# Kernel tuning notes

Measured on AMD Instinct MI355X. Metric: run time of the kernel, lower is better.

The kernel has to match this reference:

```python
import jax, jax.numpy as jnp
import numpy as np

N, E = 50000, 800000
IN_DIM, H, OUT_DIM = 128, 32, 128


def _p(key, shape, fan_in):
    return jax.random.normal(key, shape, dtype=jnp.float32) / np.float32(np.sqrt(fan_in))


def gcn(x, edge_index, W, b):
    # GCNConv with DOUBLED self-loops (outer add_self_loops + gcn_norm's own):
    # deg[i] = in_degree(i) + 2, each node receives 2*dinv[i]^2 * h[i].
    src, dst = edge_index[0], edge_index[1]
    h = x @ W  # [N, out]
    deg = jnp.zeros((x.shape[0],), h.dtype).at[dst].add(1.0) + 2.0
    dinv = jax.lax.rsqrt(deg)
    coef = dinv[src] * dinv[dst]  # [E]
    agg = jax.ops.segment_sum(h[src] * coef[:, None], dst, num_segments=x.shape[0])
    agg = agg + (2.0 * dinv * dinv)[:, None] * h
    return agg + b


def multihop(x, edge_index, W, b, fW, fb):
    # hop loop in the source always re-uses initial_x -> collapses to 1 pass
    return gcn(x, edge_index, W, b) @ fW + fb


def deconv(xc, W, b):
    # ConvTranspose1d(kernel=2, stride=2): out[n,o,2l+t] = sum_c xc[n,c,l]*W[c,o,t] + b[o]
    y = jnp.einsum('ncl,cot->nolt', xc, W) + b[None, :, None, None]
    return y.reshape(y.shape[0], y.shape[1], -1)  # [N, O, 2L]


def setup_inputs() -> dict:
    key = jax.random.key(0)
    ks = jax.random.split(key, 30)
    return {
        'x': jax.random.normal(ks[0], (N, IN_DIM), jnp.float32),
        'edge_index': jax.random.randint(ks[1], (2, E), 0, N),
        'w_enc1': _p(ks[2], (IN_DIM, H), IN_DIM), 'b_enc1': _p(ks[3], (H,), H),
        'fw_enc1': _p(ks[4], (H, H), H), 'fb_enc1': _p(ks[5], (H,), H),
        'w_enc2': _p(ks[6], (H, 2 * H), H), 'b_enc2': _p(ks[7], (2 * H,), 2 * H),
        'fw_enc2': _p(ks[8], (2 * H, 2 * H), 2 * H), 'fb_enc2': _p(ks[9], (2 * H,), 2 * H),
        'w_enc3': _p(ks[10], (2 * H, 4 * H), 2 * H), 'b_enc3': _p(ks[11], (4 * H,), 4 * H),
        'fw_enc3': _p(ks[12], (4 * H, 4 * H), 4 * H), 'fb_enc3': _p(ks[13], (4 * H,), 4 * H),
        'wd1': _p(ks[14], (4 * H, 2 * H, 2), 4 * H), 'bd1': _p(ks[15], (2 * H,), 4 * H),
        'wd2': _p(ks[16], (2 * H, H, 2), 2 * H), 'bd2': _p(ks[17], (H,), 2 * H),
        'wd3': _p(ks[18], (H, H, 2), H), 'bd3': _p(ks[19], (H,), H),
        'ws1': _p(ks[20], (2 * H, 2 * H), 2 * H), 'bs1': _p(ks[21], (2 * H,), 2 * H),
        'ws2': _p(ks[22], (H, H), H), 'bs2': _p(ks[23], (H,), H),
        'wf': _p(ks[24], (8 * H, OUT_DIM), 8 * H), 'bf': _p(ks[25], (OUT_DIM,), 8 * H),
    }


def reference(x, edge_index, w_enc1, b_enc1, fw_enc1, fb_enc1,
              w_enc2, b_enc2, fw_enc2, fb_enc2,
              w_enc3, b_enc3, fw_enc3, fb_enc3,
              wd1, bd1, wd2, bd2, wd3, bd3,
              ws1, bs1, ws2, bs2, wf, bf):
    relu = jax.nn.relu
    x1 = relu(multihop(x, edge_index, w_enc1, b_enc1, fw_enc1, fb_enc1))   # [N, H]
    x2 = relu(multihop(x1, edge_index, w_enc2, b_enc2, fw_enc2, fb_enc2))  # [N, 2H]
    x3 = relu(multihop(x2, edge_index, w_enc3, b_enc3, fw_enc3, fb_enc3))  # [N, 4H]
    d = deconv(x3[:, :, None], wd1, bd1)            # [N, 2H, 2]
    s2 = x2 @ ws1 + bs1                              # skip_conv1 (k=1) == linear
    d = d + s2[:, :, None]                           # repeat over length
    d = deconv(d, wd2, bd2)                          # [N, H, 4]
    s1 = x1 @ ws2 + bs2
    d = d + s1[:, :, None]
    d = deconv(d, wd3, bd3)                          # [N, H, 8]
    out = d.reshape(d.shape[0], -1) @ wf + bf        # [N, OUT_DIM]
    return out
```

## Files before the change

### kernel.cpp

```cpp
#include <hip/hip_runtime.h>

#define NN 50000
#define NE 800000
#define NBLK 196
#define CAP 5120

typedef _Float16 half8 __attribute__((ext_vector_type(8)));
typedef _Float16 half4 __attribute__((ext_vector_type(4)));
typedef float f32x4v __attribute__((ext_vector_type(4)));

__launch_bounds__(256)
__global__ void k_A(const int* __restrict__ srcv, const int* __restrict__ dstv,
                    int* __restrict__ bcur, unsigned int* __restrict__ epk2,
                    const float* __restrict__ wd3, const float* __restrict__ wf,
                    const float* __restrict__ w2, const float* __restrict__ fw2,
                    const float* __restrict__ w3, const float* __restrict__ fw3,
                    const float* __restrict__ b1, const float* __restrict__ fw1,
                    const float* __restrict__ fb1,
                    const float* __restrict__ b2, const float* __restrict__ fb2,
                    const float* __restrict__ b3, const float* __restrict__ fb3,
                    float* __restrict__ G,
                    float* __restrict__ Wc2, float* __restrict__ Wc3,
                    float* __restrict__ bc1, float* __restrict__ bc2,
                    float* __restrict__ bc3,
                    const float* __restrict__ w1, _Float16* __restrict__ W1pk) {
  __shared__ int cnt[256];
  __shared__ int base[256];
  int t = threadIdx.x;
  int b = blockIdx.x;
  if (b < NBLK) {
    int e0 = b * 4096;
    cnt[t] = 0;
    __syncthreads();
    unsigned int pk[16];
    int lo[16], bk[16];
    bool ok[16];
#pragma unroll
    for (int i = 0; i < 16; ++i) {
      int e = e0 + i * 256 + t;
      ok[i] = (e < NE);
      if (ok[i]) {
        int s = srcv[e], d = dstv[e];
        bk[i] = d >> 8;
        pk[i] = (unsigned int)s | ((unsigned int)(d & 255) << 16);
        lo[i] = atomicAdd(&cnt[bk[i]], 1);
      }
    }
    __syncthreads();
    int c = cnt[t];
    if (c > 0) base[t] = atomicAdd(&bcur[t], c);
    __syncthreads();
#pragma unroll
    for (int i = 0; i < 16; ++i)
      if (ok[i]) epk2[(size_t)bk[i] * CAP + base[bk[i]] + lo[i]] = pk[i];
    return;
  }
  if (b < NBLK + 105) {
    int id = (b - NBLK) * 256 + t;
    if (id < 16384) {
      int k = id & 127, r = id >> 7;
      int c = r >> 2, l = r & 3;
      float s = 0.f;
      for (int o = 0; o < 32; ++o) {
        s = fmaf(wd3[c * 64 + o * 2 + 0], wf[(o * 8 + 2 * l + 0) * 128 + k], s);
        s = fmaf(wd3[c * 64 + o * 2 + 1], wf[(o * 8 + 2 * l + 1) * 128 + k], s);
      }
      G[r * 128 + k] = s;
      return;
    }
    int id2 = id - 16384;
    if (id2 < 2048) {
      int c = id2 >> 6, k = id2 & 63;
      float s = 0.f;
      for (int j = 0; j < 64; ++j) s = fmaf(w2[c * 64 + j], fw2[j * 64 + k], s);
      Wc2[id2] = s;
    } else if (id2 < 10240) {
      int idx = id2 - 2048;
      int c = idx >> 7, k = idx & 127;
      float s = 0.f;
      for (int j = 0; j < 128; ++j) s = fmaf(w3[c * 128 + j], fw3[j * 128 + k], s);
      Wc3[idx] = s;
    } else if (id2 < 10272) {
      int k = id2 - 10240;
      float s = fb1[k];
      for (int j = 0; j < 32; ++j) s = fmaf(b1[j], fw1[j * 32 + k], s);
      bc1[k] = s;
    } else if (id2 < 10336) {
      int k = id2 - 10272;
      float s = fb2[k];
      for (int j = 0; j < 64; ++j) s = fmaf(b2[j], fw2[j * 64 + k], s);
      bc2[k] = s;
    } else if (id2 < 10464) {
      int k = id2 - 10336;
      float s = fb3[k];
      for (int j = 0; j < 128; ++j) s = fmaf(b3[j], fw3[j * 128 + k], s);
      bc3[k] = s;
    }
    return;
  }
#pragma unroll
  for (int it = 0; it < 2; ++it) {
    int id = t + it * 256;
    int l = id & 63, f = id >> 6;
    int kb = f >> 1, nb = f & 1;
    int kbase = kb * 32 + ((l >> 4) << 3);
    int col = nb * 16 + (l & 15);
#pragma unroll
    for (int j = 0; j < 8; ++j)
      W1pk[id * 8 + j] = (_Float16)w1[(kbase + j) * 32 + col];
  }
}

__launch_bounds__(256)
__global__ void k_B(const unsigned int* __restrict__ epk2, const int* __restrict__ bcur,
                    int* __restrict__ row_start, int* __restrict__ bend,
                    float* __restrict__ dinv, float* __restrict__ rdinv,
                    unsigned short* __restrict__ esrc,
                    const float* __restrict__ wd2, const float* __restrict__ G,
                    const float* __restrict__ ws2,
                    float* __restrict__ Hm, float* __restrict__ A1) {
  int t = threadIdx.x;
  int b = blockIdx.x;
  if (b < NBLK) {
    __shared__ int cnt[256];
    __shared__ int cur[256];
    __shared__ int ss[256];
    int rs0 = b * CAP;
    int count = bcur[b];
    int rs1 = rs0 + count;
    cnt[t] = 0;
    __syncthreads();
    for (int i = rs0 + t; i < rs1; i += 256) {
      unsigned int p = epk2[i];
      atomicAdd(&cnt[(p >> 16) & 255], 1);
    }
    __syncthreads();
    int d = cnt[t];
    ss[t] = d;
    __syncthreads();
    for (int off = 1; off < 256; off <<= 1) {
      int v = (t >= off) ? ss[t - off] : 0;
      __syncthreads();
      ss[t] += v;
      __syncthreads();
    }
    int rs = rs0 + ss[t] - d;
    int node = b * 256 + t;
    if (node < NN) {
      row_start[node] = rs;
      float df = (float)d + 2.0f;
      dinv[node] = rsqrtf(df);
      rdinv[node] = sqrtf(df);
    }
    if (t == 0) bend[b] = rs1;
    if (b == 0 && t == 0) row_start[NN] = NBLK * CAP;
    cur[t] = rs;
    __syncthreads();
    for (int i = rs0 + t; i < rs1; i += 256) {
      unsigned int p = epk2[i];
      int dl = (p >> 16) & 255;
      int tgt = atomicAdd(&cur[dl], 1);
      esrc[tgt] = (unsigned short)(p & 0xFFFFu);
    }
    return;
  }
  int id = (b - NBLK) * 256 + t;
  if (id < 16384) {
    int k = id & 127, r = id >> 7;
    int c = r >> 1, l = r & 1;
    float s = 0.f;
    for (int o = 0; o < 32; ++o) {
      s = fmaf(wd2[c * 64 + o * 2 + 0], G[(o * 4 + 2 * l + 0) * 128 + k], s);
      s = fmaf(wd2[c * 64 + o * 2 + 1], G[(o * 4 + 2 * l + 1) * 128 + k], s);
    }
    Hm[r * 128 + k] = s;
  } else if (id < 16384 + 4096) {
    int idx = id - 16384;
    int k = idx & 127, c = idx >> 7;
    float s = 0.f;
    for (int o = 0; o < 32; ++o) {
      float g = G[(4 * o) * 128 + k] + G[(4 * o + 1) * 128 + k] +
                G[(4 * o + 2) * 128 + k] + G[(4 * o + 3) * 128 + k];
      s = fmaf(ws2[c * 32 + o], g, s);
    }
    A1[c * 128 + k] = s;
  }
}

__device__ inline half8 cvt8f(const float* __restrict__ p) {
  float4 u = *reinterpret_cast<const float4*>(p);
  float4 v = *reinterpret_cast<const float4*>(p + 4);
  half8 a;
  a[0] = (_Float16)u.x; a[1] = (_Float16)u.y; a[2] = (_Float16)u.z; a[3] = (_Float16)u.w;
  a[4] = (_Float16)v.x; a[5] = (_Float16)v.y; a[6] = (_Float16)v.z; a[7] = (_Float16)v.w;
  return a;
}

#define NG1 782
__launch_bounds__(256)
__global__ void k_C(const float* __restrict__ X, const half8* __restrict__ W1pk,
                    const float* __restrict__ dinv, _Float16* __restrict__ Yh,
                    const float* __restrict__ wd1, const float* __restrict__ ws1,
                    const float* __restrict__ Hm, const float* __restrict__ G,
                    const float* __restrict__ wf,
                    const float* __restrict__ bd1, const float* __restrict__ bs1,
                    const float* __restrict__ bd2, const float* __restrict__ bs2,
                    const float* __restrict__ bd3, const float* __restrict__ bf,
                    float* __restrict__ A3, float* __restrict__ A2,
                    float* __restrict__ c0) {
  int t = threadIdx.x;
  int b = blockIdx.x;
  if (b < NG1) {
    int w = t >> 6, l = t & 63;
    int m16 = l & 15, g = l >> 4;
    int n0 = b * 64 + w * 16;
    int nrow = n0 + m16;
    f32x4v acc[2];
    acc[0] = (f32x4v){0.f, 0.f, 0.f, 0.f};
    acc[1] = (f32x4v){0.f, 0.f, 0.f, 0.f};
#pragma unroll
    for (int kb = 0; kb < 4; ++kb) {
      half8 a = (half8)(_Float16)0.f;
      if (nrow < NN) a = cvt8f(X + (size_t)nrow * 128 + kb * 32 + g * 8);
#pragma unroll
      for (int nb = 0; nb < 2; ++nb)
        acc[nb] = __builtin_amdgcn_mfma_f32_16x16x32_f16(a, W1pk[(kb * 2 + nb) * 64 + l],
                                                         acc[nb], 0, 0, 0);
    }
#pragma unroll
    for (int nb = 0; nb < 2; ++nb)
#pragma unroll
      for (int r = 0; r < 4; ++r) {
        int n = n0 + g * 4 + r;
        if (n < NN)
          Yh[(size_t)n * 32 + nb * 16 + m16] = (_Float16)(dinv[n] * acc[nb][r]);
      }
    return;
  }
  int id = (b - NG1) * 256 + t;
  if (id < 16384) {
    int k = id & 127, c = id >> 7;
    float s = 0.f;
    for (int j = 0; j < 128; ++j) s = fmaf(wd1[c * 128 + j], Hm[j * 128 + k], s);
    A3[c * 128 + k] = s;
  } else if (id < 16384 + 8192) {
    int idx = id - 16384;
    int k = idx & 127, c = idx >> 7;
    float s = 0.f;
    for (int o = 0; o < 64; ++o)
      s = fmaf(ws1[c * 64 + o], Hm[(2 * o) * 128 + k] + Hm[(2 * o + 1) * 128 + k], s);
    A2[c * 128 + k] = s;
  } else if (id < 16384 + 8192 + 128) {
    int k = id - 16384 - 8192;
    float s = bf[k];
    for (int o = 0; o < 64; ++o) {
      float bb = bd1[o] + bs1[o];
      s = fmaf(bb, Hm[(o * 2) * 128 + k] + Hm[(o * 2 + 1) * 128 + k], s);
    }
    for (int o = 0; o < 32; ++o) {
      float bb = bd2[o] + bs2[o];
      float g = G[(o * 4) * 128 + k] + G[(o * 4 + 1) * 128 + k] +
                G[(o * 4 + 2) * 128 + k] + G[(o * 4 + 3) * 128 + k];
      s = fmaf(bb, g, s);
    }
    for (int o = 0; o < 32; ++o) {
      float w8 = 0.f;
      for (int j = 0; j < 8; ++j) w8 += wf[(o * 8 + j) * 128 + k];
      s = fmaf(bd3[o], w8, s);
    }
    c0[k] = s;
  }
}

__device__ inline float4 gsum32h(const half4* __restrict__ H4,
                                 const unsigned short* __restrict__ esrc,
                                 const int* __restrict__ row_start,
                                 const int* __restrict__ bend,
                                 int n, int fg, int way) {
  float4 acc = make_float4(0.f, 0.f, 0.f, 0.f);
  if (way == 0) {
    half4 h = H4[(size_t)n * 8 + fg];
    acc.x = 2.f * (float)h[0]; acc.y = 2.f * (float)h[1];
    acc.z = 2.f * (float)h[2]; acc.w = 2.f * (float)h[3];
  }
  int end = min(row_start[n + 1], bend[n >> 8]);
  int i = row_start[n] + way;
  for (; i + 12 < end; i += 16) {
    int s0 = esrc[i], s1 = esrc[i + 4], s2 = esrc[i + 8], s3 = esrc[i + 12];
    half4 a = H4[(size_t)s0 * 8 + fg];
    half4 b = H4[(size_t)s1 * 8 + fg];
    half4 c = H4[(size_t)s2 * 8 + fg];
    half4 d = H4[(size_t)s3 * 8 + fg];
    acc.x += ((float)a[0] + (float)b[0]) + ((float)c[0] + (float)d[0]);
    acc.y += ((float)a[1] + (float)b[1]) + ((float)c[1] + (float)d[1]);
    acc.z += ((float)a[2] + (float)b[2]) + ((float)c[2] + (float)d[2]);
    acc.w += ((float)a[3] + (float)b[3]) + ((float)c[3] + (float)d[3]);
  }
  for (; i < end; i += 4) {
    int s = esrc[i];
    half4 a = H4[(size_t)s * 8 + fg];
    acc.x += (float)a[0]; acc.y += (float)a[1];
    acc.z += (float)a[2]; acc.w += (float)a[3];
  }
  acc.x += __shfl_xor(acc.x, 8);  acc.y += __shfl_xor(acc.y, 8);
  acc.z += __shfl_xor(acc.z, 8);  acc.w += __shfl_xor(acc.w, 8);
  acc.x += __shfl_xor(acc.x, 16); acc.y += __shfl_xor(acc.y, 16);
  acc.z += __shfl_xor(acc.z, 16); acc.w += __shfl_xor(acc.w, 16);
  return acc;
}

#define NF1 6250
__launch_bounds__(256)
__global__ void k_D(const _Float16* __restrict__ H, const unsigned short* __restrict__ esrc,
                    const int* __restrict__ row_start, const int* __restrict__ bend,
                    const float* __restrict__ dinv,
                    const float* __restrict__ W, const float* __restrict__ bias,
                    _Float16* __restrict__ Y,
                    const float* __restrict__ Wc3, const float* __restrict__ Acat,
                    _Float16* __restrict__ W3pk, _Float16* __restrict__ Apk) {
  int t = threadIdx.x;
  int b = blockIdx.x;
  if (b < NF1) {
    __shared__ float sZT[32][9];
    __shared__ float sW[32 * 32];
    int n0 = b * 8;
    {
      int kr = t >> 3, c4 = (t & 7) * 4;
      *reinterpret_cast<float4*>(&sW[kr * 32 + c4]) =
          *reinterpret_cast<const float4*>(&W[kr * 32 + c4]);
    }
    int node = t >> 5, fg = t & 7, way = (t >> 3) & 3;
    int n = n0 + node;
    float4 z = gsum32h(reinterpret_cast<const half4*>(H), esrc, row_start, bend, n, fg, way);
    if (way == 0) {
      float dv = dinv[n];
      sZT[fg * 4 + 0][node] = dv * z.x;
      sZT[fg * 4 + 1][node] = dv * z.y;
      sZT[fg * 4 + 2][node] = dv * z.z;
      sZT[fg * 4 + 3][node] = dv * z.w;
    }
    __syncthreads();
    int nd = t >> 5, col = t & 31;
    float a = bias[col];
#pragma unroll
    for (int k = 0; k < 32; ++k) a = fmaf(sZT[k][nd], sW[k * 32 + col], a);
    Y[(size_t)(n0 + nd) * 32 + col] = (_Float16)(dinv[n0 + nd] * fmaxf(a, 0.f));
    return;
  }
  int id = (b - NF1) * 256 + t;
  if (id < 1024) {
    int l = id & 63, nb = (id >> 6) & 7, kb = id >> 9;
    int kbase = kb * 32 + ((l >> 4) << 3);
    int col = nb * 16 + (l & 15);
#pragma unroll
    for (int j = 0; j < 8; ++j)
      W3pk[id * 8 + j] = (_Float16)Wc3[(kbase + j) * 128 + col];
  } else if (id < 1024 + 3584) {
    int idx = id - 1024;
    int l = idx & 63, nb = (idx >> 6) & 7, kb = idx >> 9;
    int kbase = kb * 32 + ((l >> 4) << 3);
    int col = nb * 16 + (l & 15);
#pragma unroll
    for (int j = 0; j < 8; ++j)
      Apk[idx * 8 + j] = (_Float16)Acat[(kbase + j) * 128 + col];
  }
}

__launch_bounds__(256)
__global__ void k_fuse2(const _Float16* __restrict__ H, const unsigned short* __restrict__ esrc,
                        const int* __restrict__ row_start, const int* __restrict__ bend,
                        const float* __restrict__ dinv,
                        const float* __restrict__ W, const float* __restrict__ bias,
                        _Float16* __restrict__ Y) {
  __shared__ float sZT[32][9];
  __shared__ float sW[32 * 64];
  int t = threadIdx.x;
  int n0 = blockIdx.x * 8;
#pragma unroll
  for (int it = 0; it < 2; ++it) {
    int idx = t + it * 256;
    int kr = idx >> 4, c4 = (idx & 15) * 4;
    *reinterpret_cast<float4*>(&sW[kr * 64 + c4]) =
        *reinterpret_cast<const float4*>(&W[kr * 64 + c4]);
  }
  int node = t >> 5, fg = t & 7, way = (t >> 3) & 3;
  int n = n0 + node;
  float4 z = gsum32h(reinterpret_cast<const half4*>(H), esrc, row_start, bend, n, fg, way);
  if (way == 0) {
    float dv = dinv[n];
    sZT[fg * 4 + 0][node] = dv * z.x;
    sZT[fg * 4 + 1][node] = dv * z.y;
    sZT[fg * 4 + 2][node] = dv * z.z;
    sZT[fg * 4 + 3][node] = dv * z.w;
  }
  __syncthreads();
  int nd = t >> 5, col = t & 31;
  float a = bias[col], b = bias[col + 32];
#pragma unroll
  for (int k = 0; k < 32; ++k) {
    float zv = sZT[k][nd];
    a = fmaf(zv, sW[k * 64 + col], a);
    b = fmaf(zv, sW[k * 64 + col + 32], b);
  }
  float dv = dinv[n0 + nd];
  Y[(size_t)(n0 + nd) * 64 + col] = (_Float16)(dv * fmaxf(a, 0.f));
  Y[(size_t)(n0 + nd) * 64 + col + 32] = (_Float16)(dv * fmaxf(b, 0.f));
}

__launch_bounds__(256)
__global__ void k_gath64(const _Float16* __restrict__ H, const unsigned short* __restrict__ esrc,
                         const int* __restrict__ row_start, const int* __restrict__ bend,
                         const float* __restrict__ dinv, _Float16* __restrict__ Zh) {
  int t = threadIdx.x;
  int n = blockIdx.x * 4 + (t >> 6);
  int fg = t & 15, way = (t >> 4) & 3;
  const half4* H4 = reinterpret_cast<const half4*>(H);
  float4 acc = make_float4(0.f, 0.f, 0.f, 0.f);
  if (way == 0) {
    half4 h = H4[(size_t)n * 16 + fg];
    acc.x = 2.f * (float)h[0]; acc.y = 2.f * (float)h[1];
    acc.z = 2.f * (float)h[2]; acc.w = 2.f * (float)h[3];
  }
  int end = min(row_start[n + 1], bend[n >> 8]);
  int i = row_start[n] + way;
  for (; i + 12 < end; i += 16) {
    int s0 = esrc[i], s1 = esrc[i + 4], s2 = esrc[i + 8], s3 = esrc[i + 12];
    half4 a = H4[(size_t)s0 * 16 + fg];
    half4 b = H4[(size_t)s1 * 16 + fg];
    half4 c = H4[(size_t)s2 * 16 + fg];
    half4 d = H4[(size_t)s3 * 16 + fg];
    acc.x += ((float)a[0] + (float)b[0]) + ((float)c[0] + (float)d[0]);
    acc.y += ((float)a[1] + (float)b[1]) + ((float)c[1] + (float)d[1]);
    acc.z += ((float)a[2] + (float)b[2]) + ((float)c[2] + (float)d[2]);
    acc.w += ((float)a[3] + (float)b[3]) + ((float)c[3] + (float)d[3]);
  }
  for (; i < end; i += 4) {
    int s = esrc[i];
    half4 a = H4[(size_t)s * 16 + fg];
    acc.x += (float)a[0]; acc.y += (float)a[1];
    acc.z += (float)a[2]; acc.w += (float)a[3];
  }
  acc.x += __shfl_xor(acc.x, 16); acc.y += __shfl_xor(acc.y, 16);
  acc.z += __shfl_xor(acc.z, 16); acc.w += __shfl_xor(acc.w, 16);
  acc.x += __shfl_xor(acc.x, 32); acc.y += __shfl_xor(acc.y, 32);
  acc.z += __shfl_xor(acc.z, 32); acc.w += __shfl_xor(acc.w, 32);
  if (way == 0) {
    float dv = dinv[n];
    half4 hv;
    hv[0] = (_Float16)(dv * acc.x); hv[1] = (_Float16)(dv * acc.y);
    hv[2] = (_Float16)(dv * acc.z); hv[3] = (_Float16)(dv * acc.w);
    *reinterpret_cast<half4*>(Zh + (size_t)n * 64 + fg * 4) = hv;
  }
}

__device__ inline half8 cvt8h(const _Float16* __restrict__ p, float s) {
  half8 v = *reinterpret_cast<const half8*>(p);
  half8 a;
#pragma unroll
  for (int i = 0; i < 8; ++i) a[i] = (_Float16)(s * (float)v[i]);
  return a;
}

__launch_bounds__(256)
__global__ void k_decode(const _Float16* __restrict__ z3h, const _Float16* __restrict__ X2h,
                         const _Float16* __restrict__ X1h, const float* __restrict__ rdinv,
                         const half8* __restrict__ W3pk, const half8* __restrict__ Apk,
                         const float* __restrict__ bc3, const float* __restrict__ c0,
                         float* __restrict__ out) {
  __shared__ _Float16 sX3[4][16][136];
  int t = threadIdx.x;
  int w = t >> 6, l = t & 63;
  int m16 = l & 15, g = l >> 4;
  int n0 = blockIdx.x * 64 + w * 16;
  int nrow = n0 + m16;

  f32x4v acc[8];
#pragma unroll
  for (int nb = 0; nb < 8; ++nb) {
    float bv = bc3[nb * 16 + m16];
    acc[nb] = (f32x4v){bv, bv, bv, bv};
  }
#pragma unroll
  for (int kb = 0; kb < 2; ++kb) {
    half8 a = *reinterpret_cast<const half8*>(z3h + (size_t)nrow * 64 + kb * 32 + g * 8);
#pragma unroll
    for (int nb = 0; nb < 8; ++nb) {
      half8 b = W3pk[(kb * 8 + nb) * 64 + l];
      acc[nb] = __builtin_amdgcn_mfma_f32_16x16x32_f16(a, b, acc[nb], 0, 0, 0);
    }
  }
#pragma unroll
  for (int nb = 0; nb < 8; ++nb)
#pragma unroll
    for (int r = 0; r < 4; ++r)
      sX3[w][g * 4 + r][nb * 16 + m16] = (_Float16)fmaxf(acc[nb][r], 0.0f);
  __syncthreads();

  float rd = rdinv[nrow];
#pragma unroll
  for (int nb = 0; nb < 8; ++nb) {
    float cv = c0[nb * 16 + m16];
    acc[nb] = (f32x4v){cv, cv, cv, cv};
  }
#pragma unroll
  for (int kb = 0; kb < 7; ++kb) {
    half8 a;
    if (kb < 4)
      a = *reinterpret_cast<const half8*>(&sX3[w][m16][kb * 32 + g * 8]);
    else if (kb < 6)
      a = cvt8h(X2h + (size_t)nrow * 64 + (kb - 4) * 32 + g * 8, rd);
    else
      a = cvt8h(X1h + (size_t)nrow * 32 + g * 8, rd);
#pragma unroll
    for (int nb = 0; nb < 8; ++nb) {
      half8 b = Apk[(kb * 8 + nb) * 64 + l];
      acc[nb] = __builtin_amdgcn_mfma_f32_16x16x32_f16(a, b, acc[nb], 0, 0, 0);
    }
  }
#pragma unroll
  for (int nb = 0; nb < 8; ++nb)
#pragma unroll
    for (int r = 0; r < 4; ++r) {
      int n = n0 + g * 4 + r;
      if (n < NN) out[(size_t)n * 128 + nb * 16 + m16] = acc[nb][r];
    }
}

extern "C" void kernel_launch(void* const* d_in, const int* in_sizes, int n_in,
                              void* d_out, int out_size, void* d_ws, size_t ws_size,
                              hipStream_t stream) {
  const float* x   = (const float*)d_in[0];
  const int* ei    = (const int*)d_in[1];
  const int* srcv  = ei;
  const int* dstv  = ei + NE;
  const float* w1  = (const float*)d_in[2];
  const float* b1  = (const float*)d_in[3];
  const float* fw1 = (const float*)d_in[4];
  const float* fb1 = (const float*)d_in[5];
  const float* w2  = (const float*)d_in[6];
  const float* b2  = (const float*)d_in[7];
  const float* fw2 = (const float*)d_in[8];
  const float* fb2 = (const float*)d_in[9];
  const float* w3  = (const float*)d_in[10];
  const float* b3  = (const float*)d_in[11];
  const float* fw3 = (const float*)d_in[12];
  const float* fb3 = (const float*)d_in[13];
  const float* wd1 = (const float*)d_in[14];
  const float* bd1 = (const float*)d_in[15];
  const float* wd2 = (const float*)d_in[16];
  const float* bd2 = (const float*)d_in[17];
  const float* wd3 = (const float*)d_in[18];
  const float* bd3 = (const float*)d_in[19];
  const float* ws1 = (const float*)d_in[20];
  const float* bs1 = (const float*)d_in[21];
  const float* ws2 = (const float*)d_in[22];
  const float* bs2 = (const float*)d_in[23];
  const float* wf  = (const float*)d_in[24];
  const float* bf  = (const float*)d_in[25];

  float* fp = (float*)d_ws;
  float* dinv = fp;
  float* rdinv= dinv + 50176;
  _Float16* h1h = (_Float16*)(rdinv + 50176);
  _Float16* x1h = h1h + 1601536;
  _Float16* x2h = x1h + 1601536;
  _Float16* z3h = x2h + 3203072;
  float* Wc2  = (float*)(z3h + 3203072);
  float* Wc3  = Wc2 + 2048;
  float* bc1  = Wc3 + 8192;
  float* bc2  = bc1 + 64;
  float* bc3  = bc2 + 64;
  float* G    = bc3 + 128;
  float* Hm   = G + 16384;
  float* A3   = Hm + 16384;
  float* A2   = A3 + 16384;
  float* A1   = A2 + 8192;
  float* c0   = A1 + 4096;
  _Float16* W3pk = (_Float16*)(c0 + 256);
  _Float16* Apk  = W3pk + 8192;
  _Float16* W1pk = Apk + 28672;
  unsigned int* epk2 = (unsigned int*)(W1pk + 4096);
  unsigned short* esrc = (unsigned short*)(epk2 + NBLK * CAP);
  int* ip     = (int*)(esrc + NBLK * CAP);
  int* row_start = ip;
  int* bend   = row_start + 50176;
  int* bcur   = bend + 256;

  float* outp = (float*)d_out;

  hipMemsetAsync(bcur, 0, NBLK * sizeof(int), stream);
  k_A<<<NBLK + 105 + 1, 256, 0, stream>>>(srcv, dstv, bcur, epk2,
                                          wd3, wf, w2, fw2, w3, fw3, b1, fw1, fb1,
                                          b2, fb2, b3, fb3, G, Wc2, Wc3, bc1, bc2, bc3,
                                          w1, W1pk);
  k_B<<<NBLK + 80, 256, 0, stream>>>(epk2, bcur, row_start, bend, dinv, rdinv, esrc,
                                     wd2, G, ws2, Hm, A1);
  k_C<<<NG1 + 97, 256, 0, stream>>>(x, (const half8*)W1pk, dinv, h1h,
                                    wd1, ws1, Hm, G, wf, bd1, bs1, bd2, bs2, bd3, bf,
                                    A3, A2, c0);
  k_D<<<NF1 + 18, 256, 0, stream>>>(h1h, esrc, row_start, bend, dinv, fw1, bc1, x1h,
                                    Wc3, A3 , W3pk, Apk);
  k_fuse2<<<NN / 8, 256, 0, stream>>>(x1h, esrc, row_start, bend, dinv, Wc2, bc2, x2h);
  k_gath64<<<NN / 4, 256, 0, stream>>>(x2h, esrc, row_start, bend, dinv, z3h);
  k_decode<<<(NN + 63) / 64, 256, 0, stream>>>(z3h, x2h, x1h, rdinv, (const half8*)W3pk,
                                               (const half8*)Apk, bc3, c0, outp);
}
```

Measured before the change: 139.7 us.

## Fuse 64-wide aggregation into decode kernel and widen gathers to half8

Removes the separate k_gath64 kernel and its z3h intermediate. The third-layer neighbor aggregation is now computed inside k_decode into shared memory before the MFMA stage. k_D and k_fuse2 switch from half4 to half8 gathers with a different lane-to-edge mapping, and k_fuse2 processes 4 nodes per block with 64 threads each. This saves one launch and an HBM round trip of the aggregated features. In exchange, decode does serial per-node gathers with only 4 threads per node, which may expose latency and load imbalance.

```diff
diff --git a/kernel.cpp b/kernel.cpp
--- a/kernel.cpp
+++ b/kernel.cpp
@@ -272,43 +272,6 @@
   }
 }
 
-__device__ inline float4 gsum32h(const half4* __restrict__ H4,
-                                 const unsigned short* __restrict__ esrc,
-                                 const int* __restrict__ row_start,
-                                 const int* __restrict__ bend,
-                                 int n, int fg, int way) {
-  float4 acc = make_float4(0.f, 0.f, 0.f, 0.f);
-  if (way == 0) {
-    half4 h = H4[(size_t)n * 8 + fg];
-    acc.x = 2.f * (float)h[0]; acc.y = 2.f * (float)h[1];
-    acc.z = 2.f * (float)h[2]; acc.w = 2.f * (float)h[3];
-  }
-  int end = min(row_start[n + 1], bend[n >> 8]);
-  int i = row_start[n] + way;
-  for (; i + 12 < end; i += 16) {
-    int s0 = esrc[i], s1 = esrc[i + 4], s2 = esrc[i + 8], s3 = esrc[i + 12];
-    half4 a = H4[(size_t)s0 * 8 + fg];
-    half4 b = H4[(size_t)s1 * 8 + fg];
-    half4 c = H4[(size_t)s2 * 8 + fg];
-    half4 d = H4[(size_t)s3 * 8 + fg];
-    acc.x += ((float)a[0] + (float)b[0]) + ((float)c[0] + (float)d[0]);
-    acc.y += ((float)a[1] + (float)b[1]) + ((float)c[1] + (float)d[1]);
-    acc.z += ((float)a[2] + (float)b[2]) + ((float)c[2] + (float)d[2]);
-    acc.w += ((float)a[3] + (float)b[3]) + ((float)c[3] + (float)d[3]);
-  }
-  for (; i < end; i += 4) {
-    int s = esrc[i];
-    half4 a = H4[(size_t)s * 8 + fg];
-    acc.x += (float)a[0]; acc.y += (float)a[1];
-    acc.z += (float)a[2]; acc.w += (float)a[3];
-  }
-  acc.x += __shfl_xor(acc.x, 8);  acc.y += __shfl_xor(acc.y, 8);
-  acc.z += __shfl_xor(acc.z, 8);  acc.w += __shfl_xor(acc.w, 8);
-  acc.x += __shfl_xor(acc.x, 16); acc.y += __shfl_xor(acc.y, 16);
-  acc.z += __shfl_xor(acc.z, 16); acc.w += __shfl_xor(acc.w, 16);
-  return acc;
-}
-
 #define NF1 6250
 __launch_bounds__(256)
 __global__ void k_D(const _Float16* __restrict__ H, const unsigned short* __restrict__ esrc,
@@ -329,15 +292,42 @@
       *reinterpret_cast<float4*>(&sW[kr * 32 + c4]) =
           *reinterpret_cast<const float4*>(&W[kr * 32 + c4]);
     }
-    int node = t >> 5, fg = t & 7, way = (t >> 3) & 3;
+    int node = t >> 5, sub = t & 31, fg = sub & 3, way = sub >> 2;
     int n = n0 + node;
-    float4 z = gsum32h(reinterpret_cast<const half4*>(H), esrc, row_start, bend, n, fg, way);
+    const half8* H8 = reinterpret_cast<const half8*>(H);
+    float acc[8];
+#pragma unroll
+    for (int j = 0; j < 8; ++j) acc[j] = 0.f;
+    if (way == 0) {
+      half8 h = H8[(size_t)n * 4 + fg];
+#pragma unroll
+      for (int j = 0; j < 8; ++j) acc[j] = 2.f * (float)h[j];
+    }
+    int end = min(row_start[n + 1], bend[n >> 8]);
+    int i = row_start[n] + way;
+    for (; i + 8 < end; i += 16) {
+      int s0 = esrc[i], s1 = esrc[i + 8];
+      half8 a = H8[(size_t)s0 * 4 + fg];
+      half8 bb = H8[(size_t)s1 * 4 + fg];
+#pragma unroll
+      for (int j = 0; j < 8; ++j) acc[j] += (float)a[j] + (float)bb[j];
+    }
+    for (; i < end; i += 8) {
+      int s = esrc[i];
+      half8 a = H8[(size_t)s * 4 + fg];
+#pragma unroll
+      for (int j = 0; j < 8; ++j) acc[j] += (float)a[j];
+    }
+#pragma unroll
+    for (int j = 0; j < 8; ++j) {
+      acc[j] += __shfl_xor(acc[j], 4);
+      acc[j] += __shfl_xor(acc[j], 8);
+      acc[j] += __shfl_xor(acc[j], 16);
+    }
     if (way == 0) {
       float dv = dinv[n];
-      sZT[fg * 4 + 0][node] = dv * z.x;
-      sZT[fg * 4 + 1][node] = dv * z.y;
-      sZT[fg * 4 + 2][node] = dv * z.z;
-      sZT[fg * 4 + 3][node] = dv * z.w;
+#pragma unroll
+      for (int j = 0; j < 8; ++j) sZT[fg * 8 + j][node] = dv * acc[j];
     }
     __syncthreads();
     int nd = t >> 5, col = t & 31;
@@ -372,10 +362,10 @@
                         const float* __restrict__ dinv,
                         const float* __restrict__ W, const float* __restrict__ bias,
                         _Float16* __restrict__ Y) {
-  __shared__ float sZT[32][9];
+  __shared__ float sZT[32][5];
   __shared__ float sW[32 * 64];
   int t = threadIdx.x;
-  int n0 = blockIdx.x * 8;
+  int n0 = blockIdx.x * 4;
 #pragma unroll
   for (int it = 0; it < 2; ++it) {
     int idx = t + it * 256;
@@ -383,74 +373,43 @@
     *reinterpret_cast<float4*>(&sW[kr * 64 + c4]) =
         *reinterpret_cast<const float4*>(&W[kr * 64 + c4]);
   }
-  int node = t >> 5, fg = t & 7, way = (t >> 3) & 3;
+  int node = t >> 6, sub = t & 63, fg = sub & 3, way = (sub >> 2) & 7, dup = sub >> 5;
   int n = n0 + node;
-  float4 z = gsum32h(reinterpret_cast<const half4*>(H), esrc, row_start, bend, n, fg, way);
-  if (way == 0) {
+  const half8* H8 = reinterpret_cast<const half8*>(H);
+  float acc[8];
+#pragma unroll
+  for (int j = 0; j < 8; ++j) acc[j] = 0.f;
+  if (way == 0 && dup == 0) {
+    half8 h = H8[(size_t)n * 4 + fg];
+#pragma unroll
+    for (int j = 0; j < 8; ++j) acc[j] = 2.f * (float)h[j];
+  }
+  int end = min(row_start[n + 1], bend[n >> 8]);
+  int i = row_start[n] + way + dup * 8;
+  for (; i < end; i += 16) {
+    int s = esrc[i];
+    half8 a = H8[(size_t)s * 4 + fg];
+#pragma unroll
+    for (int j = 0; j < 8; ++j) acc[j] += (float)a[j];
+  }
+#pragma unroll
+  for (int j = 0; j < 8; ++j) {
+    acc[j] += __shfl_xor(acc[j], 4);
+    acc[j] += __shfl_xor(acc[j], 8);
+    acc[j] += __shfl_xor(acc[j], 16);
+    acc[j] += __shfl_xor(acc[j], 32);
+  }
+  if (sub < 4) {
     float dv = dinv[n];
-    sZT[fg * 4 + 0][node] = dv * z.x;
-    sZT[fg * 4 + 1][node] = dv * z.y;
-    sZT[fg * 4 + 2][node] = dv * z.z;
-    sZT[fg * 4 + 3][node] = dv * z.w;
+#pragma unroll
+    for (int j = 0; j < 8; ++j) sZT[fg * 8 + j][node] = dv * acc[j];
   }
   __syncthreads();
-  int nd = t >> 5, col = t & 31;
-  float a = bias[col], b = bias[col + 32];
-#pragma unroll
-  for (int k = 0; k < 32; ++k) {
-    float zv = sZT[k][nd];
-    a = fmaf(zv, sW[k * 64 + col], a);
-    b = fmaf(zv, sW[k * 64 + col + 32], b);
-  }
-  float dv = dinv[n0 + nd];
-  Y[(size_t)(n0 + nd) * 64 + col] = (_Float16)(dv * fmaxf(a, 0.f));
-  Y[(size_t)(n0 + nd) * 64 + col + 32] = (_Float16)(dv * fmaxf(b, 0.f));
-}
-
-__launch_bounds__(256)
-__global__ void k_gath64(const _Float16* __restrict__ H, const unsigned short* __restrict__ esrc,
-                         const int* __restrict__ row_start, const int* __restrict__ bend,
-                         const float* __restrict__ dinv, _Float16* __restrict__ Zh) {
-  int t = threadIdx.x;
-  int n = blockIdx.x * 4 + (t >> 6);
-  int fg = t & 15, way = (t >> 4) & 3;
-  const half4* H4 = reinterpret_cast<const half4*>(H);
-  float4 acc = make_float4(0.f, 0.f, 0.f, 0.f);
-  if (way == 0) {
-    half4 h = H4[(size_t)n * 16 + fg];
-    acc.x = 2.f * (float)h[0]; acc.y = 2.f * (float)h[1];
-    acc.z = 2.f * (float)h[2]; acc.w = 2.f * (float)h[3];
-  }
-  int end = min(row_start[n + 1], bend[n >> 8]);
-  int i = row_start[n] + way;
-  for (; i + 12 < end; i += 16) {
-    int s0 = esrc[i], s1 = esrc[i + 4], s2 = esrc[i + 8], s3 = esrc[i + 12];
-    half4 a = H4[(size_t)s0 * 16 + fg];
-    half4 b = H4[(size_t)s1 * 16 + fg];
-    half4 c = H4[(size_t)s2 * 16 + fg];
-    half4 d = H4[(size_t)s3 * 16 + fg];
-    acc.x += ((float)a[0] + (float)b[0]) + ((float)c[0] + (float)d[0]);
-    acc.y += ((float)a[1] + (float)b[1]) + ((float)c[1] + (float)d[1]);
-    acc.z += ((float)a[2] + (float)b[2]) + ((float)c[2] + (float)d[2]);
-    acc.w += ((float)a[3] + (float)b[3]) + ((float)c[3] + (float)d[3]);
-  }
-  for (; i < end; i += 4) {
-    int s = esrc[i];
-    half4 a = H4[(size_t)s * 16 + fg];
-    acc.x += (float)a[0]; acc.y += (float)a[1];
-    acc.z += (float)a[2]; acc.w += (float)a[3];
-  }
-  acc.x += __shfl_xor(acc.x, 16); acc.y += __shfl_xor(acc.y, 16);
-  acc.z += __shfl_xor(acc.z, 16); acc.w += __shfl_xor(acc.w, 16);
-  acc.x += __shfl_xor(acc.x, 32); acc.y += __shfl_xor(acc.y, 32);
-  acc.z += __shfl_xor(acc.z, 32); acc.w += __shfl_xor(acc.w, 32);
-  if (way == 0) {
-    float dv = dinv[n];
-    half4 hv;
-    hv[0] = (_Float16)(dv * acc.x); hv[1] = (_Float16)(dv * acc.y);
-    hv[2] = (_Float16)(dv * acc.z); hv[3] = (_Float16)(dv * acc.w);
-    *reinterpret_cast<half4*>(Zh + (size_t)n * 64 + fg * 4) = hv;
-  }
+  int nd = t >> 6, col = t & 63;
+  float a = bias[col];
+#pragma unroll
+  for (int k = 0; k < 32; ++k) a = fmaf(sZT[k][nd], sW[k * 64 + col], a);
+  Y[(size_t)(n0 + nd) * 64 + col] = (_Float16)(dinv[n0 + nd] * fmaxf(a, 0.f));
 }
 
 __device__ inline half8 cvt8h(const _Float16* __restrict__ p, float s) {
@@ -462,13 +421,70 @@
 }
 
 __launch_bounds__(256)
-__global__ void k_decode(const _Float16* __restrict__ z3h, const _Float16* __restrict__ X2h,
-                         const _Float16* __restrict__ X1h, const float* __restrict__ rdinv,
+__global__ void k_decode(const _Float16* __restrict__ X2h, const _Float16* __restrict__ X1h,
+                         const unsigned short* __restrict__ esrc,
+                         const int* __restrict__ row_start, const int* __restrict__ bend,
+                         const float* __restrict__ dinv, const float* __restrict__ rdinv,
                          const half8* __restrict__ W3pk, const half8* __restrict__ Apk,
                          const float* __restrict__ bc3, const float* __restrict__ c0,
                          float* __restrict__ out) {
+  __shared__ _Float16 zT[64][72];
   __shared__ _Float16 sX3[4][16][136];
   int t = threadIdx.x;
+
+  {
+    int ln = t >> 2, q = t & 3;
+    int n = blockIdx.x * 64 + ln;
+    float acc[16];
+#pragma unroll
+    for (int j = 0; j < 16; ++j) acc[j] = 0.f;
+    if (n < NN) {
+      const half8* H8 = reinterpret_cast<const half8*>(X2h);
+      half8 h0 = H8[(size_t)n * 8 + q * 2];
+      half8 h1 = H8[(size_t)n * 8 + q * 2 + 1];
+#pragma unroll
+      for (int j = 0; j < 8; ++j) {
+        acc[j] = 2.f * (float)h0[j];
+        acc[8 + j] = 2.f * (float)h1[j];
+      }
+      int end = min(row_start[n + 1], bend[n >> 8]);
+      int i = row_start[n];
+      for (; i + 3 < end; i += 4) {
+        int s0 = esrc[i], s1 = esrc[i + 1], s2 = esrc[i + 2], s3 = esrc[i + 3];
+        half8 a0 = H8[(size_t)s0 * 8 + q * 2], a1 = H8[(size_t)s0 * 8 + q * 2 + 1];
+        half8 b0 = H8[(size_t)s1 * 8 + q * 2], b1 = H8[(size_t)s1 * 8 + q * 2 + 1];
+        half8 c0v = H8[(size_t)s2 * 8 + q * 2], c1v = H8[(size_t)s2 * 8 + q * 2 + 1];
+        half8 d0 = H8[(size_t)s3 * 8 + q * 2], d1 = H8[(size_t)s3 * 8 + q * 2 + 1];
+#pragma unroll
+        for (int j = 0; j < 8; ++j) {
+          acc[j] += ((float)a0[j] + (float)b0[j]) + ((float)c0v[j] + (float)d0[j]);
+          acc[8 + j] += ((float)a1[j] + (float)b1[j]) + ((float)c1v[j] + (float)d1[j]);
+        }
+      }
+      for (; i < end; ++i) {
+        int s = esrc[i];
+        half8 a0 = H8[(size_t)s * 8 + q * 2], a1 = H8[(size_t)s * 8 + q * 2 + 1];
+#pragma unroll
+        for (int j = 0; j < 8; ++j) {
+          acc[j] += (float)a0[j];
+          acc[8 + j] += (float)a1[j];
+        }
+      }
+      float dv = dinv[n];
+#pragma unroll
+      for (int j = 0; j < 16; ++j) acc[j] *= dv;
+    }
+    half8 z0, z1;
+#pragma unroll
+    for (int j = 0; j < 8; ++j) {
+      z0[j] = (_Float16)acc[j];
+      z1[j] = (_Float16)acc[8 + j];
+    }
+    *reinterpret_cast<half8*>(&zT[ln][q * 16]) = z0;
+    *reinterpret_cast<half8*>(&zT[ln][q * 16 + 8]) = z1;
+  }
+  __syncthreads();
+
   int w = t >> 6, l = t & 63;
   int m16 = l & 15, g = l >> 4;
   int n0 = blockIdx.x * 64 + w * 16;
@@ -482,7 +498,7 @@
   }
 #pragma unroll
   for (int kb = 0; kb < 2; ++kb) {
-    half8 a = *reinterpret_cast<const half8*>(z3h + (size_t)nrow * 64 + kb * 32 + g * 8);
+    half8 a = *reinterpret_cast<const half8*>(&zT[w * 16 + m16][kb * 32 + g * 8]);
 #pragma unroll
     for (int nb = 0; nb < 8; ++nb) {
       half8 b = W3pk[(kb * 8 + nb) * 64 + l];
@@ -564,8 +580,7 @@
   _Float16* h1h = (_Float16*)(rdinv + 50176);
   _Float16* x1h = h1h + 1601536;
   _Float16* x2h = x1h + 1601536;
-  _Float16* z3h = x2h + 3203072;
-  float* Wc2  = (float*)(z3h + 3203072);
+  float* Wc2  = (float*)(x2h + 3203072);
   float* Wc3  = Wc2 + 2048;
   float* bc1  = Wc3 + 8192;
   float* bc2  = bc1 + 64;
@@ -600,8 +615,8 @@
                                     A3, A2, c0);
   k_D<<<NF1 + 18, 256, 0, stream>>>(h1h, esrc, row_start, bend, dinv, fw1, bc1, x1h,
                                     Wc3, A3 , W3pk, Apk);
-  k_fuse2<<<NN / 8, 256, 0, stream>>>(x1h, esrc, row_start, bend, dinv, Wc2, bc2, x2h);
-  k_gath64<<<NN / 4, 256, 0, stream>>>(x2h, esrc, row_start, bend, dinv, z3h);
-  k_decode<<<(NN + 63) / 64, 256, 0, stream>>>(z3h, x2h, x1h, rdinv, (const half8*)W3pk,
+  k_fuse2<<<NN / 4, 256, 0, stream>>>(x1h, esrc, row_start, bend, dinv, Wc2, bc2, x2h);
+  k_decode<<<(NN + 63) / 64, 256, 0, stream>>>(x2h, x1h, esrc, row_start, bend, dinv,
+                                               rdinv, (const half8*)W3pk,
                                                (const half8*)Apk, bc3, c0, outp);
 }
```

Result: no change. 141.2 us (+1.1%).
